# Kernel optimization log

Measured on AMD Instinct MI355X. Metric: run time of the kernel, lower is better.

The kernel has to match this reference:

```python
import jax, jax.numpy as jnp
import numpy as np

B, L, E = 8, 2048, 128


def setup_inputs() -> dict:
    key = jax.random.key(0)
    k1, k2, k3, k4 = jax.random.split(key, 4)
    return {
        "Uq": jax.random.normal(k1, (B, L, E), dtype=jnp.float32),
        "Uid": jax.random.normal(k2, (B, L, E), dtype=jnp.float32),
        "mask": jnp.ones((L, L), dtype=jnp.float32),
        "Wc_w": jax.random.normal(k3, (3 * E,), dtype=jnp.float32) * 0.05,
        "Wc_b": jax.random.normal(k4, (), dtype=jnp.float32) * 0.05,
    }


def reference(Uq, Uid, mask, Wc_w, Wc_b):
    # Wc(cat(Uid, Uq, Uid*Uq)) decomposed into three direct projections —
    # exact same math as the Linear over the concatenation, never
    # materializing the [B, L, L, 3E] tensor.
    e = Uq.shape[-1]
    w_id, w_q, w_mul = Wc_w[:e], Wc_w[e:2 * e], Wc_w[2 * e:]
    s_id = jnp.einsum("bie,e->bi", Uid, w_id)          # [B, Lid]
    s_q = jnp.einsum("bje,e->bj", Uq, w_q)             # [B, Lq]
    s_mul = jnp.einsum("bie,bje,e->bij", Uid, Uq, w_mul)  # [B, Lid, Lq]
    S = (s_id[:, :, None] + s_q[:, None, :] + s_mul + Wc_b) * mask
    # S_D2Q = Softmax(dim=0) over the per-example [Lid, Lq] matrix -> axis=1
    P = jax.nn.softmax(S, axis=1)                      # [B, Lid, Lq]
    A_D2Q = jnp.einsum("bij,bje->bie", P, Uq)          # [B, Lid, E]
    M = jnp.einsum("bij,bkj->bik", P, P)               # P @ P^T, [B, Lid, Lid]
    A_Q2D = jnp.einsum("bik,bke->bie", M, Uid)         # [B, Lid, E]
    Vid = jnp.concatenate([Uid, A_D2Q, Uid * A_D2Q, Uid * A_Q2D], axis=-1)
    return Vid  # [B, Lid, 4E]
```

## Files before the change

kernel.cpp:

```cpp
#include <hip/hip_runtime.h>

#define L 2048
#define E 128
#define NB 8

typedef float f32x4 __attribute__((ext_vector_type(4)));
typedef short short8 __attribute__((ext_vector_type(8)));
typedef unsigned int u32;

static __device__ inline float bf2f(ushort u) {
  union { float f; u32 i; } v; v.i = ((u32)u) << 16; return v.f;
}
static __device__ inline ushort f2bf(float f) {
  union { float f; u32 i; } v; v.f = f;
  u32 x = v.i;
  return (ushort)((x + 0x7fffu + ((x >> 16) & 1u)) >> 16);
}

__device__ inline void glds16(const ushort* g, ushort* l) {
  __builtin_amdgcn_global_load_lds(
      (const __attribute__((address_space(1))) u32*)(const void*)g,
      (__attribute__((address_space(3))) u32*)(void*)l, 16, 0, 0);
}

__global__ __launch_bounds__(128) void k_prep(const float* __restrict__ Uq,
                                              const float* __restrict__ Uid,
                                              const float* __restrict__ Wcw,
                                              ushort* __restrict__ UqB,
                                              ushort* __restrict__ UidB,
                                              ushort* __restrict__ Uidw,
                                              float* __restrict__ s_id,
                                              float* __restrict__ s_q) {
  int r = blockIdx.x;
  int e = threadIdx.x;
  ushort uqu  = f2bf(Uq[(long)r * E + e]);
  ushort uidu = f2bf(Uid[(long)r * E + e]);
  float uqf = bf2f(uqu), uidf = bf2f(uidu);
  float wid  = bf2f(f2bf(Wcw[e]));
  float wq   = bf2f(f2bf(Wcw[E + e]));
  float wmul = bf2f(f2bf(Wcw[2 * E + e]));
  UqB[(long)r * E + e]  = uqu;
  UidB[(long)r * E + e] = uidu;
  Uidw[(long)r * E + e] = f2bf(uidf * wmul);
  float sid = uidf * wid, sq = uqf * wq;
  #pragma unroll
  for (int off = 32; off >= 1; off >>= 1) {
    sid += __shfl_down(sid, off, 64);
    sq  += __shfl_down(sq,  off, 64);
  }
  __shared__ float red[4];
  int wv = threadIdx.x >> 6;
  if ((threadIdx.x & 63) == 0) { red[wv * 2] = sid; red[wv * 2 + 1] = sq; }
  __syncthreads();
  if (threadIdx.x == 0) { s_id[r] = red[0] + red[2]; s_q[r] = red[1] + red[3]; }
}

__global__ __launch_bounds__(256) void k_maskT(const float* __restrict__ mask,
                                               ushort* __restrict__ maskT) {
  __shared__ ushort tile[32][33];
  int j0 = blockIdx.x * 32, i0 = blockIdx.y * 32;
  int tx = threadIdx.x, ty = threadIdx.y;
  #pragma unroll
  for (int r = ty; r < 32; r += 8)
    tile[r][tx] = f2bf(mask[(long)(i0 + r) * L + j0 + tx]);
  __syncthreads();
  #pragma unroll
  for (int r = ty; r < 32; r += 8)
    maskT[(long)(j0 + r) * L + i0 + tx] = tile[tx][r];
}

__global__ __launch_bounds__(256) void k_tr2(const ushort* __restrict__ s1,
                                             ushort* __restrict__ d1,
                                             const ushort* __restrict__ s2,
                                             ushort* __restrict__ d2) {
  __shared__ ushort tile[32][33];
  int zz = blockIdx.z;
  long base = (long)(zz & (NB - 1)) * L * E;
  const ushort* src = ((zz < NB) ? s1 : s2) + base;
  ushort* dst = ((zz < NB) ? d1 : d2) + base;
  int c0 = blockIdx.x * 32, r0 = blockIdx.y * 32;
  int tx = threadIdx.x, ty = threadIdx.y;
  #pragma unroll
  for (int i = ty; i < 32; i += 8)
    tile[i][tx] = src[(long)(r0 + i) * E + c0 + tx];
  __syncthreads();
  #pragma unroll
  for (int i = ty; i < 32; i += 8)
    dst[(long)(c0 + i) * L + r0 + tx] = tile[tx][i];
}

__device__ inline void gemm128_loop(const ushort* __restrict__ A,
                                    const ushort* __restrict__ B,
                                    long ldA, long ldB, int K,
                                    f32x4 acc[4][4],
                                    ushort* ldsA, ushort* ldsB) {
  const int t = threadIdx.x;
  const int w = t >> 6, lane = t & 63;
  const int mrow = lane & 15, quad = lane >> 4;
  const int lr = lane >> 3;
  const int lc = ((lane & 7) ^ lr) * 8;
  const int mh = (w & 1) * 64, nh = (w >> 1) * 64;
  for (int k0 = 0; k0 < K; k0 += 64) {
    __syncthreads();
    #pragma unroll
    for (int s = 0; s < 4; s++) {
      int row = w * 32 + s * 8 + lr;
      glds16(&A[(long)row * ldA + k0 + lc], &ldsA[w * 2048 + s * 512]);
      glds16(&B[(long)row * ldB + k0 + lc], &ldsB[w * 2048 + s * 512]);
    }
    __syncthreads();
    #pragma unroll
    for (int kk = 0; kk < 2; kk++) {
      short8 av[4], bv[4];
      #pragma unroll
      for (int mi = 0; mi < 4; mi++)
        av[mi] = *(const short8*)&ldsA[(mh + mi * 16 + mrow) * 64 +
                                       ((kk * 32 + quad * 8) ^ ((mrow & 7) << 3))];
      #pragma unroll
      for (int ni = 0; ni < 4; ni++)
        bv[ni] = *(const short8*)&ldsB[(nh + ni * 16 + mrow) * 64 +
                                       ((kk * 32 + quad * 8) ^ ((mrow & 7) << 3))];
      #pragma unroll
      for (int mi = 0; mi < 4; mi++)
        #pragma unroll
        for (int ni = 0; ni < 4; ni++)
          acc[mi][ni] = __builtin_amdgcn_mfma_f32_16x16x32_bf16(av[mi], bv[ni], acc[mi][ni], 0, 0, 0);
    }
  }
}

__device__ inline void gemm64x128_loop(const ushort* __restrict__ A,
                                       const ushort* __restrict__ B,
                                       long ldA, long ldB, int K,
                                       f32x4 acc[2][4],
                                       ushort* ldsA, ushort* ldsB) {
  const int t = threadIdx.x;
  const int w = t >> 6, lane = t & 63;
  const int mrow = lane & 15, quad = lane >> 4;
  const int lr = lane >> 3;
  const int lc = ((lane & 7) ^ lr) * 8;
  const int mh = (w & 1) * 32, nh = (w >> 1) * 64;
  for (int k0 = 0; k0 < K; k0 += 64) {
    __syncthreads();
    #pragma unroll
    for (int s = 0; s < 2; s++) {
      int row = w * 16 + s * 8 + lr;
      glds16(&A[(long)row * ldA + k0 + lc], &ldsA[w * 1024 + s * 512]);
    }
    #pragma unroll
    for (int s = 0; s < 4; s++) {
      int row = w * 32 + s * 8 + lr;
      glds16(&B[(long)row * ldB + k0 + lc], &ldsB[w * 2048 + s * 512]);
    }
    __syncthreads();
    #pragma unroll
    for (int kk = 0; kk < 2; kk++) {
      short8 av[2], bv[4];
      #pragma unroll
      for (int mi = 0; mi < 2; mi++)
        av[mi] = *(const short8*)&ldsA[(mh + mi * 16 + mrow) * 64 +
                                       ((kk * 32 + quad * 8) ^ ((mrow & 7) << 3))];
      #pragma unroll
      for (int ni = 0; ni < 4; ni++)
        bv[ni] = *(const short8*)&ldsB[(nh + ni * 16 + mrow) * 64 +
                                       ((kk * 32 + quad * 8) ^ ((mrow & 7) << 3))];
      #pragma unroll
      for (int mi = 0; mi < 2; mi++)
        #pragma unroll
        for (int ni = 0; ni < 4; ni++)
          acc[mi][ni] = __builtin_amdgcn_mfma_f32_16x16x32_bf16(av[mi], bv[ni], acc[mi][ni], 0, 0, 0);
    }
  }
}

__global__ __launch_bounds__(256) void k_scores(const ushort* __restrict__ Uq,
                                                const ushort* __restrict__ Uidw,
                                                const float* __restrict__ s_id,
                                                const float* __restrict__ s_q,
                                                const float* __restrict__ Wcb,
                                                const ushort* __restrict__ maskT,
                                                ushort* __restrict__ St,
                                                float* __restrict__ ps, int b0) {
  __shared__ ushort lds[16384];
  ushort* ldsA = lds;
  ushort* ldsB = lds + 8192;
  int bz = blockIdx.z, b = b0 + bz;
  int m0 = blockIdx.x * 128;
  int n0 = blockIdx.y * 128;
  int tile_i = blockIdx.y;
  const ushort* A = Uq   + (long)b * L * E + (long)m0 * E;
  const ushort* B = Uidw + (long)b * L * E + (long)n0 * E;
  f32x4 acc[4][4] = {};
  gemm128_loop(A, B, E, E, E, acc, ldsA, ldsB);
  float bias = bf2f(f2bf(Wcb[0]));
  const int t = threadIdx.x, w = t >> 6, lane = t & 63;
  const int col = lane & 15, quad = lane >> 4;
  const int mh = (w & 1) * 64, nh = (w >> 1) * 64;

  __syncthreads();
  float sidv[4];
  #pragma unroll
  for (int ni = 0; ni < 4; ni++)
    sidv[ni] = s_id[b * L + n0 + nh + ni * 16 + col];
  #pragma unroll
  for (int mi = 0; mi < 4; mi++) {
    float sqv[4];
    #pragma unroll
    for (int rg = 0; rg < 4; rg++)
      sqv[rg] = s_q[b * L + m0 + mh + mi * 16 + quad * 4 + rg];
    #pragma unroll
    for (int ni = 0; ni < 4; ni++) {
      int cl = nh + ni * 16 + col;
      #pragma unroll
      for (int rg = 0; rg < 4; rg++) {
        int row = mh + mi * 16 + quad * 4 + rg;
        float v = acc[mi][ni][rg] + sqv[rg] + sidv[ni] + bias;
        lds[row * 128 + (cl ^ ((row & 7) << 3))] = f2bf(v);
      }
    }
  }
  __syncthreads();
  #pragma unroll
  for (int p = 0; p < 8; p++) {
    int r2 = p * 16 + (t >> 4);
    int cu = (t & 15) * 8;
    uint4 sv = *(const uint4*)&lds[r2 * 128 + (cu ^ ((r2 & 7) << 3))];
    int jg = m0 + r2;
    uint4 mv = *(const uint4*)&maskT[(long)jg * L + n0 + cu];
    ushort o[8];
    float lsum = 0.f;
    const ushort* sp = (const ushort*)&sv;
    const ushort* mp = (const ushort*)&mv;
    #pragma unroll
    for (int k = 0; k < 8; k++) {
      float ev = __expf(bf2f(sp[k]) * bf2f(mp[k]));
      o[k] = f2bf(ev);
      lsum += bf2f(o[k]);
    }
    *(uint4*)&St[(long)bz * L * L + (long)jg * L + n0 + cu] = *(const uint4*)&o[0];
    #pragma unroll
    for (int off = 8; off >= 1; off >>= 1) lsum += __shfl_xor(lsum, off, 64);
    if ((t & 15) == 0) {
      ps[((long)bz * L + jg) * 16 + tile_i] = lsum;
    }
  }
}

__global__ __launch_bounds__(256) void k_redstats(const float* __restrict__ ps,
                                                  float* __restrict__ lg) {
  int idx = blockIdx.x * 256 + threadIdx.x;
  const float* psr = ps + (long)idx * 16;
  float s = 0.f;
  #pragma unroll
  for (int k = 0; k < 16; k++) s += psr[k];
  lg[idx] = 1.0f / s;
}

__global__ __launch_bounds__(256) void k_ptr(const ushort* __restrict__ St,
                                             ushort* __restrict__ P,
                                             const float* __restrict__ lg) {
  __shared__ ushort tl[4 * 1056];
  int bz = blockIdx.y;
  int t = threadIdx.x, wid = t >> 6, lane = t & 63;
  int flat = blockIdx.x * 4 + wid;
  int j0 = (flat >> 6) * 32;
  int i0 = (flat & 63) * 32;
  const ushort* Sb = St + (long)bz * L * L;
  ushort* Pb = P  + (long)bz * L * L;
  ushort* wt = tl + wid * 1056;
  int r = lane >> 1, c0 = (lane & 1) * 16;
  float inv = lg[bz * L + j0 + r];
  const ushort* src = Sb + (long)(j0 + r) * L + i0 + c0;
  uint4 q0 = *(const uint4*)src;
  uint4 q1 = *(const uint4*)(src + 8);
  ushort o[16];
  const ushort* pr = (const ushort*)&q0;
  #pragma unroll
  for (int k = 0; k < 8; k++) o[k] = f2bf(bf2f(pr[k]) * inv);
  pr = (const ushort*)&q1;
  #pragma unroll
  for (int k = 0; k < 8; k++) o[8 + k] = f2bf(bf2f(pr[k]) * inv);
  #pragma unroll
  for (int k = 0; k < 16; k++) wt[(c0 + k) * 33 + r] = o[k];
  asm volatile("s_waitcnt lgkmcnt(0)" ::: "memory");
  __builtin_amdgcn_sched_barrier(0);
  ushort po[16];
  #pragma unroll
  for (int k = 0; k < 16; k++) po[k] = wt[r * 33 + c0 + k];
  ushort* pd = Pb + (long)(i0 + r) * L + j0 + c0;
  *(uint4*)pd       = *(const uint4*)&po[0];
  *(uint4*)(pd + 8) = *(const uint4*)&po[8];
}

__global__ __launch_bounds__(256) void k_gemm_Tt(const ushort* __restrict__ UidT,
                                                 const ushort* __restrict__ Et,
                                                 const float* __restrict__ lg,
                                                 ushort* __restrict__ Tt, int b0) {
  __shared__ ushort lds[12288];
  ushort* ldsA = lds;
  ushort* ldsB = lds + 4096;
  int bz = blockIdx.z, b = b0 + bz;
  int e0 = (blockIdx.x & 1) * 64;
  int j0 = (blockIdx.x >> 1) * 128;
  const ushort* A = UidT + (long)b * E * L + (long)e0 * L;
  const ushort* B = Et   + (long)bz * L * L + (long)j0 * L;
  f32x4 acc[2][4] = {};
  gemm64x128_loop(A, B, L, L, L, acc, ldsA, ldsB);
  const int t = threadIdx.x, w = t >> 6, lane = t & 63;
  const int col = lane & 15, quad = lane >> 4;
  const int mh = (w & 1) * 32, nh = (w >> 1) * 64;
  __syncthreads();
  #pragma unroll
  for (int mi = 0; mi < 2; mi++)
    #pragma unroll
    for (int ni = 0; ni < 4; ni++) {
      int cl = nh + ni * 16 + col;
      float sc = lg[(long)bz * L + j0 + cl];
      #pragma unroll
      for (int rg = 0; rg < 4; rg++) {
        int row = mh + mi * 16 + quad * 4 + rg;
        lds[row * 128 + (cl ^ ((row & 7) << 3))] = f2bf(acc[mi][ni][rg] * sc);
      }
    }
  __syncthreads();
  #pragma unroll
  for (int p = 0; p < 4; p++) {
    int r2 = p * 16 + (t >> 4);
    int cu = (t & 15) * 8;
    uint4 v = *(const uint4*)&lds[r2 * 128 + (cu ^ ((r2 & 7) << 3))];
    *(uint4*)&Tt[(long)b * E * L + (long)(e0 + r2) * L + j0 + cu] = v;
  }
}

__global__ __launch_bounds__(256) void k_gemm_A(const ushort* __restrict__ P,
                                                const ushort* __restrict__ UqT,
                                                const ushort* __restrict__ Tt,
                                                const ushort* __restrict__ UidB,
                                                float* __restrict__ out, int b0) {
  __shared__ ushort ldsA[64 * 64];
  __shared__ ushort ldsB[128 * 64];
  int bz = blockIdx.z, b = b0 + bz;
  int m0 = blockIdx.x * 64;
  int n0 = blockIdx.y * 128;
  const ushort* A = P + (long)bz * L * L + (long)m0 * L;
  const ushort* B = (blockIdx.y == 0) ? (UqT + (long)b * E * L)
                                      : (Tt  + (long)b * E * L);
  f32x4 acc[2][4] = {};
  gemm64x128_loop(A, B, L, L, L, acc, ldsA, ldsB);
  const int t = threadIdx.x, w = t >> 6, lane = t & 63;
  const int col = lane & 15, quad = lane >> 4;
  const int mh = (w & 1) * 32, nh = (w >> 1) * 64;
  #pragma unroll
  for (int mi = 0; mi < 2; mi++)
    #pragma unroll
    for (int ni = 0; ni < 4; ni++)
      #pragma unroll
      for (int rg = 0; rg < 4; rg++) {
        int ig = m0 + mh + mi * 16 + quad * 4 + rg;
        int c  = n0 + nh + ni * 16 + col;
        float a = acc[mi][ni][rg];
        float uidf = bf2f(UidB[(long)b * L * E + (long)ig * E + (c & 127)]);
        long ob = ((long)b * L + ig) * 512;
        if (c < 128) {
          out[ob + c]       = uidf;
          out[ob + 128 + c] = a;
          out[ob + 256 + c] = uidf * a;
        } else {
          out[ob + 256 + c] = uidf * a;
        }
      }
}

extern "C" void kernel_launch(void* const* d_in, const int* in_sizes, int n_in,
                              void* d_out, int out_size, void* d_ws, size_t ws_size,
                              hipStream_t stream) {
  const float* Uq   = (const float*)d_in[0];
  const float* Uid  = (const float*)d_in[1];
  const float* mask = (const float*)d_in[2];
  const float* Wcw  = (const float*)d_in[3];
  const float* Wcb  = (const float*)d_in[4];
  float* out = (float*)d_out;

  char* ws = (char*)d_ws;
  size_t off = 0;
  auto alloc = [&](size_t bytes) -> void* {
    void* p = ws + off; off += (bytes + 255) & ~(size_t)255; return p;
  };
  const size_t nUb = (size_t)NB * L * E * 2;
  ushort* UqB   = (ushort*)alloc(nUb);
  ushort* UidB  = (ushort*)alloc(nUb);
  ushort* Uidw  = (ushort*)alloc(nUb);
  ushort* UqT   = (ushort*)alloc(nUb);
  ushort* UidT  = (ushort*)alloc(nUb);
  ushort* Tt    = (ushort*)alloc(nUb);
  ushort* maskT = (ushort*)alloc((size_t)L * L * 2);
  float*  s_id  = (float*)alloc((size_t)NB * L * 4);
  float*  s_q   = (float*)alloc((size_t)NB * L * 4);
  float*  lg    = (float*)alloc((size_t)NB * L * 4);
  float*  ps    = (float*)alloc((size_t)NB * L * 16 * 4);
  const size_t per_batch = (size_t)L * L * 2;
  size_t avail = (ws_size > off + 2 * per_batch) ? (ws_size - off) : 2 * per_batch;
  int nb_c = (int)(avail / (2 * per_batch));
  if (nb_c < 1) nb_c = 1;
  if (nb_c > NB) nb_c = NB;
  ushort* St = (ushort*)(ws + off);
  ushort* P  = (ushort*)(ws + off + nb_c * per_batch);

  dim3 tb(32, 8);
  k_prep<<<NB * L, E, 0, stream>>>(Uq, Uid, Wcw, UqB, UidB, Uidw, s_id, s_q);
  k_maskT<<<dim3(L / 32, L / 32), tb, 0, stream>>>(mask, maskT);
  k_tr2<<<dim3(E / 32, L / 32, 2 * NB), tb, 0, stream>>>(UqB, UqT, UidB, UidT);

  for (int b0 = 0; b0 < NB; b0 += nb_c) {
    int nb = (NB - b0 < nb_c) ? (NB - b0) : nb_c;
    k_scores<<<dim3(L / 128, L / 128, nb), 256, 0, stream>>>(UqB, Uidw, s_id, s_q, Wcb, maskT, St, ps, b0);
    k_redstats<<<dim3(nb * L / 256), 256, 0, stream>>>(ps, lg);
    k_ptr<<<dim3((L / 32) * (L / 32) / 4, nb), 256, 0, stream>>>(St, P, lg);
    k_gemm_Tt<<<dim3(2 * (L / 128), 1, nb), 256, 0, stream>>>(UidT, St, lg, Tt, b0);
    k_gemm_A<<<dim3(L / 64, 2, nb), 256, 0, stream>>>(P, UqT, Tt, UidB, out, b0);
  }
}
```

Baseline: 224.5 us.

## Fuse normalize-and-transpose of P into the A-GEMM operand load

Removes the separate k_ptr kernel, which read the unnormalized transposed scores, scaled them by the inverse column sums and wrote a transposed bf16 P matrix. k_gemm_A now reads the transposed scores directly, scales them on the fly, and transposes them into a swizzled, padded LDS tile as its A operand, with register prefetch of the next slice. This drops a full L×L bf16 write and read per batch and halves the workspace needed per batch, so more batches fit per chunk. In exchange the GEMM's A path uses scalar LDS stores and per-element conversions instead of async global-to-LDS loads.

```diff
diff --git a/kernel.cpp b/kernel.cpp
--- a/kernel.cpp
+++ b/kernel.cpp
@@ -256,42 +256,6 @@
   lg[idx] = 1.0f / s;
 }
 
-__global__ __launch_bounds__(256) void k_ptr(const ushort* __restrict__ St,
-                                             ushort* __restrict__ P,
-                                             const float* __restrict__ lg) {
-  __shared__ ushort tl[4 * 1056];
-  int bz = blockIdx.y;
-  int t = threadIdx.x, wid = t >> 6, lane = t & 63;
-  int flat = blockIdx.x * 4 + wid;
-  int j0 = (flat >> 6) * 32;
-  int i0 = (flat & 63) * 32;
-  const ushort* Sb = St + (long)bz * L * L;
-  ushort* Pb = P  + (long)bz * L * L;
-  ushort* wt = tl + wid * 1056;
-  int r = lane >> 1, c0 = (lane & 1) * 16;
-  float inv = lg[bz * L + j0 + r];
-  const ushort* src = Sb + (long)(j0 + r) * L + i0 + c0;
-  uint4 q0 = *(const uint4*)src;
-  uint4 q1 = *(const uint4*)(src + 8);
-  ushort o[16];
-  const ushort* pr = (const ushort*)&q0;
-  #pragma unroll
-  for (int k = 0; k < 8; k++) o[k] = f2bf(bf2f(pr[k]) * inv);
-  pr = (const ushort*)&q1;
-  #pragma unroll
-  for (int k = 0; k < 8; k++) o[8 + k] = f2bf(bf2f(pr[k]) * inv);
-  #pragma unroll
-  for (int k = 0; k < 16; k++) wt[(c0 + k) * 33 + r] = o[k];
-  asm volatile("s_waitcnt lgkmcnt(0)" ::: "memory");
-  __builtin_amdgcn_sched_barrier(0);
-  ushort po[16];
-  #pragma unroll
-  for (int k = 0; k < 16; k++) po[k] = wt[r * 33 + c0 + k];
-  ushort* pd = Pb + (long)(i0 + r) * L + j0 + c0;
-  *(uint4*)pd       = *(const uint4*)&po[0];
-  *(uint4*)(pd + 8) = *(const uint4*)&po[8];
-}
-
 __global__ __launch_bounds__(256) void k_gemm_Tt(const ushort* __restrict__ UidT,
                                                  const ushort* __restrict__ Et,
                                                  const float* __restrict__ lg,
@@ -332,24 +296,78 @@
   }
 }
 
-__global__ __launch_bounds__(256) void k_gemm_A(const ushort* __restrict__ P,
+__global__ __launch_bounds__(256) void k_gemm_A(const ushort* __restrict__ Et,
                                                 const ushort* __restrict__ UqT,
                                                 const ushort* __restrict__ Tt,
                                                 const ushort* __restrict__ UidB,
+                                                const float* __restrict__ lg,
                                                 float* __restrict__ out, int b0) {
-  __shared__ ushort ldsA[64 * 64];
+  __shared__ ushort ldsA[64 * 72];
   __shared__ ushort ldsB[128 * 64];
   int bz = blockIdx.z, b = b0 + bz;
   int m0 = blockIdx.x * 64;
   int n0 = blockIdx.y * 128;
-  const ushort* A = P + (long)bz * L * L + (long)m0 * L;
+  const ushort* Eb = Et + (long)bz * L * L + m0;
+  const float* lgb = lg + (long)bz * L;
   const ushort* B = (blockIdx.y == 0) ? (UqT + (long)b * E * L)
                                       : (Tt  + (long)b * E * L);
+  const int t = threadIdx.x, w = t >> 6, lane = t & 63;
+  const int mrow = lane & 15, quad = lane >> 4;
+  const int lr = lane >> 3;
+  const int lc = ((lane & 7) ^ lr) * 8;
+  const int mh = (w & 1) * 32, nh = (w >> 1) * 64;
+  const int jp2 = (t >> 3) * 2;
+  const int ic  = (t & 7) * 8;
   f32x4 acc[2][4] = {};
-  gemm64x128_loop(A, B, L, L, L, acc, ldsA, ldsB);
-  const int t = threadIdx.x, w = t >> 6, lane = t & 63;
-  const int col = lane & 15, quad = lane >> 4;
-  const int mh = (w & 1) * 32, nh = (w >> 1) * 64;
+  uint4 q0 = *(const uint4*)&Eb[(long)jp2 * L + ic];
+  uint4 q1 = *(const uint4*)&Eb[(long)(jp2 + 1) * L + ic];
+  float s0 = lgb[jp2], s1 = lgb[jp2 + 1];
+  for (int k0 = 0; k0 < L; k0 += 64) {
+    __syncthreads();
+    #pragma unroll
+    for (int s = 0; s < 4; s++) {
+      int row = w * 32 + s * 8 + lr;
+      glds16(&B[(long)row * L + k0 + lc], &ldsB[w * 2048 + s * 512]);
+    }
+    {
+      const ushort* p0 = (const ushort*)&q0;
+      const ushort* p1 = (const ushort*)&q1;
+      #pragma unroll
+      for (int k = 0; k < 8; k++) {
+        u32 pk = (u32)f2bf(bf2f(p0[k]) * s0) |
+                 ((u32)f2bf(bf2f(p1[k]) * s1) << 16);
+        int i = ic + k;
+        int cs = jp2 ^ (((i >> 3) & 7) << 3);
+        *(u32*)&ldsA[i * 72 + cs] = pk;
+      }
+    }
+    __syncthreads();
+    if (k0 + 64 < L) {
+      q0 = *(const uint4*)&Eb[(long)(k0 + 64 + jp2) * L + ic];
+      q1 = *(const uint4*)&Eb[(long)(k0 + 64 + jp2 + 1) * L + ic];
+      s0 = lgb[k0 + 64 + jp2]; s1 = lgb[k0 + 64 + jp2 + 1];
+    }
+    #pragma unroll
+    for (int kk = 0; kk < 2; kk++) {
+      short8 av[2], bv[4];
+      #pragma unroll
+      for (int mi = 0; mi < 2; mi++) {
+        int i = mh + mi * 16 + mrow;
+        av[mi] = *(const short8*)&ldsA[i * 72 +
+                   ((kk * 32 + quad * 8) ^ (((i >> 3) & 7) << 3))];
+      }
+      #pragma unroll
+      for (int ni = 0; ni < 4; ni++)
+        bv[ni] = *(const short8*)&ldsB[(nh + ni * 16 + mrow) * 64 +
+                                       ((kk * 32 + quad * 8) ^ ((mrow & 7) << 3))];
+      #pragma unroll
+      for (int mi = 0; mi < 2; mi++)
+        #pragma unroll
+        for (int ni = 0; ni < 4; ni++)
+          acc[mi][ni] = __builtin_amdgcn_mfma_f32_16x16x32_bf16(av[mi], bv[ni], acc[mi][ni], 0, 0, 0);
+    }
+  }
+  const int col = mrow;
   #pragma unroll
   for (int mi = 0; mi < 2; mi++)
     #pragma unroll
@@ -399,12 +417,11 @@
   float*  lg    = (float*)alloc((size_t)NB * L * 4);
   float*  ps    = (float*)alloc((size_t)NB * L * 16 * 4);
   const size_t per_batch = (size_t)L * L * 2;
-  size_t avail = (ws_size > off + 2 * per_batch) ? (ws_size - off) : 2 * per_batch;
-  int nb_c = (int)(avail / (2 * per_batch));
+  size_t avail = (ws_size > off + per_batch) ? (ws_size - off) : per_batch;
+  int nb_c = (int)(avail / per_batch);
   if (nb_c < 1) nb_c = 1;
   if (nb_c > NB) nb_c = NB;
   ushort* St = (ushort*)(ws + off);
-  ushort* P  = (ushort*)(ws + off + nb_c * per_batch);
 
   dim3 tb(32, 8);
   k_prep<<<NB * L, E, 0, stream>>>(Uq, Uid, Wcw, UqB, UidB, Uidw, s_id, s_q);
@@ -415,8 +432,7 @@
     int nb = (NB - b0 < nb_c) ? (NB - b0) : nb_c;
     k_scores<<<dim3(L / 128, L / 128, nb), 256, 0, stream>>>(UqB, Uidw, s_id, s_q, Wcb, maskT, St, ps, b0);
     k_redstats<<<dim3(nb * L / 256), 256, 0, stream>>>(ps, lg);
-    k_ptr<<<dim3((L / 32) * (L / 32) / 4, nb), 256, 0, stream>>>(St, P, lg);
     k_gemm_Tt<<<dim3(2 * (L / 128), 1, nb), 256, 0, stream>>>(UidT, St, lg, Tt, b0);
-    k_gemm_A<<<dim3(L / 64, 2, nb), 256, 0, stream>>>(P, UqT, Tt, UidB, out, b0);
-  }
-}
+    k_gemm_A<<<dim3(L / 64, 2, nb), 256, 0, stream>>>(St, UqT, Tt, UidB, lg, out, b0);
+  }
+}
```

Result: faster. 204.7 us (-8.8%).
